# Performance work log

Measured on AMD Instinct MI355X. Metric: run time of the kernel, lower is better.

The kernel has to match this reference:

```python
import jax, jax.numpy as jnp
import numpy as np

NUM_HEADS = 32
NUM_KV_HEADS = 8
HEAD_DIM = 64

def rotate_half(x):
    x1, x2 = jnp.split(x, 2, axis=-1)
    return jnp.concatenate((-x2, x1), axis=-1)

def setup_inputs() -> dict:
    key = jax.random.key(0)
    ks = jax.random.split(key, 7)
    B, S, H = 1, 2048, 2048
    hidden_states = jax.random.normal(ks[0], (B, S, H), dtype=jnp.float32)
    # RoPE tables (llama-style) for positions 0..S-1
    inv_freq = 1.0 / (10000.0 ** (np.arange(0, HEAD_DIM, 2, dtype=np.float32) / HEAD_DIM))
    t = np.arange(S, dtype=np.float32)
    freqs = np.outer(t, inv_freq)              # [S, HEAD_DIM//2]
    emb = np.concatenate([freqs, freqs], axis=-1)  # [S, HEAD_DIM]
    cos = jnp.asarray(np.cos(emb)[None], dtype=jnp.float32)  # [1, S, HEAD_DIM]
    sin = jnp.asarray(np.sin(emb)[None], dtype=jnp.float32)
    sc = 0.02
    Wq = jax.random.normal(ks[1], (H, H), dtype=jnp.float32) * sc
    Wk = jax.random.normal(ks[2], (NUM_KV_HEADS * HEAD_DIM, H), dtype=jnp.float32) * sc
    Wv = jax.random.normal(ks[3], (NUM_KV_HEADS * HEAD_DIM, H), dtype=jnp.float32) * sc
    Wo = jax.random.normal(ks[4], (H, H), dtype=jnp.float32) * sc
    return {"hidden_states": hidden_states, "cos": cos, "sin": sin,
            "Wq": Wq, "Wk": Wk, "Wv": Wv, "Wo": Wo}

def reference(hidden_states, cos, sin, Wq, Wk, Wv, Wo):
    B, S, H = hidden_states.shape
    nh, nkv, hd = NUM_HEADS, NUM_KV_HEADS, HEAD_DIM
    n_rep = nh // nkv
    # projections (torch Linear: x @ W.T)
    q = (hidden_states @ Wq.T).reshape(B, S, nh, hd).transpose(0, 2, 1, 3)   # [B,nh,S,hd]
    k = (hidden_states @ Wk.T).reshape(B, S, nkv, hd).transpose(0, 2, 1, 3)  # [B,nkv,S,hd]
    v = (hidden_states @ Wv.T).reshape(B, S, nkv, hd).transpose(0, 2, 1, 3)
    # RoPE: cos/sin [B,S,hd] -> broadcast over heads
    c = cos[:, None, :, :]
    s = sin[:, None, :, :]
    q = q * c + rotate_half(q) * s
    k = k * c + rotate_half(k) * s
    # GQA: repeat_interleave kv heads
    k = jnp.repeat(k, n_rep, axis=1)  # [B,nh,S,hd]
    v = jnp.repeat(v, n_rep, axis=1)
    # eager attention (NOTE: source applies no causal mask)
    scores = jnp.einsum('bhqd,bhkd->bhqk', q, k) / jnp.sqrt(jnp.float32(hd))
    attn = jax.nn.softmax(scores.astype(jnp.float32), axis=-1).astype(q.dtype)
    out = jnp.einsum('bhqk,bhkd->bhqd', attn, v)          # [B,nh,S,hd]
    out = out.transpose(0, 2, 1, 3).reshape(B, S, nh * hd)
    return out @ Wo.T
```

## Files before the change

kernel.cpp:

```cpp
#include <hip/hip_runtime.h>

typedef __bf16 bf16;
typedef __bf16 bf16x8 __attribute__((ext_vector_type(8)));
typedef __bf16 bf16x4 __attribute__((ext_vector_type(4)));
typedef float f32x4 __attribute__((ext_vector_type(4)));

__device__ __forceinline__ void gload_lds16(const void* g, void* l) {
  __builtin_amdgcn_global_load_lds(
      (const __attribute__((address_space(1))) void*)g,
      (__attribute__((address_space(3))) void*)l, 16, 0, 0);
}

__global__ __launch_bounds__(256) void cast_all(const float* __restrict__ hs,
                                                const float* __restrict__ Wq,
                                                const float* __restrict__ Wk,
                                                const float* __restrict__ Wv,
                                                const float* __restrict__ Wo,
                                                bf16* __restrict__ hsb,
                                                bf16* __restrict__ Wqkv,
                                                bf16* __restrict__ Wob) {
  long i = (long)blockIdx.x * 256 + threadIdx.x;
  const float* s; bf16* d;
  if (i < 1048576)      { s = hs + i * 4;                 d = hsb  + i * 4; }
  else if (i < 2097152) { s = Wq + (i - 1048576) * 4;     d = Wqkv + (i - 1048576) * 4; }
  else if (i < 2359296) { s = Wk + (i - 2097152) * 4;     d = Wqkv + 4194304 + (i - 2097152) * 4; }
  else if (i < 2621440) { s = Wv + (i - 2359296) * 4;     d = Wqkv + 5242880 + (i - 2359296) * 4; }
  else                  { s = Wo + (i - 2621440) * 4;     d = Wob  + (i - 2621440) * 4; }
  float4 v = *(const float4*)s;
  bf16x4 o;
  o[0] = (bf16)v.x; o[1] = (bf16)v.y; o[2] = (bf16)v.z; o[3] = (bf16)v.w;
  *(bf16x4*)d = o;
}

__global__ __launch_bounds__(256) void gemm_qkv(const bf16* __restrict__ A,
                                                const bf16* __restrict__ B,
                                                const float* __restrict__ cosb,
                                                const float* __restrict__ sinb,
                                                bf16* __restrict__ QK,
                                                bf16* __restrict__ Vt_g,
                                                int K) {
  __shared__ bf16 As[2][64][64];
  __shared__ bf16 Bs[2][128][64];
  const int tid  = threadIdx.x;
  const int lane = tid & 63;
  const int w    = tid >> 6;
  const int m0 = blockIdx.y * 64;
  const int n0 = blockIdx.x * 128;
  const int wr = w >> 1, wc = w & 1;
  const int l15 = lane & 15, lq = lane >> 4;

  f32x4 acc[2][4] = {};

  const bf16* Ag = A + (long)(m0 + w * 16 + (lane >> 3)) * K + ((lane & 7) << 3);
  const bf16* Bg = B + (long)(n0 + w * 32 + (lane >> 3)) * K + ((lane & 7) << 3);

#pragma unroll
  for (int i = 0; i < 2; ++i)
    gload_lds16(Ag + (long)i * 8 * K, &As[0][w * 16 + i * 8][0]);
#pragma unroll
  for (int i = 0; i < 4; ++i)
    gload_lds16(Bg + (long)i * 8 * K, &Bs[0][w * 32 + i * 8][0]);
  __syncthreads();

  int cur = 0;
  for (int k0 = 0; k0 < K; k0 += 64) {
    if (k0 + 64 < K) {
#pragma unroll
      for (int i = 0; i < 2; ++i)
        gload_lds16(Ag + (long)i * 8 * K + k0 + 64, &As[cur ^ 1][w * 16 + i * 8][0]);
#pragma unroll
      for (int i = 0; i < 4; ++i)
        gload_lds16(Bg + (long)i * 8 * K + k0 + 64, &Bs[cur ^ 1][w * 32 + i * 8][0]);
    }
#pragma unroll
    for (int kk = 0; kk < 64; kk += 32) {
      bf16x8 a[2], b[4];
#pragma unroll
      for (int m = 0; m < 2; ++m)
        a[m] = *(const bf16x8*)&As[cur][wr * 32 + m * 16 + l15][kk + (lq << 3)];
#pragma unroll
      for (int n = 0; n < 4; ++n)
        b[n] = *(const bf16x8*)&Bs[cur][wc * 64 + n * 16 + l15][kk + (lq << 3)];
#pragma unroll
      for (int m = 0; m < 2; ++m)
#pragma unroll
        for (int n = 0; n < 4; ++n)
          acc[m][n] = __builtin_amdgcn_mfma_f32_16x16x32_bf16(a[m], b[n], acc[m][n], 0, 0, 0);
    }
    __syncthreads();
    cur ^= 1;
  }

  const int rb = m0 + wr * 32 + (lq << 2);
  if (n0 >= 2560) {
    const int cb = n0 + wc * 64 + l15;
#pragma unroll
    for (int m = 0; m < 2; ++m)
#pragma unroll
      for (int n = 0; n < 4; ++n)
#pragma unroll
        for (int j = 0; j < 4; ++j)
          Vt_g[(long)(cb + n * 16 - 2560) * 2048 + (rb + m * 16 + j)] = (bf16)acc[m][n][j];
  } else {
    const int colb = n0 + wc * 64;
    const float scale = (colb >> 6) < 32 ? 0.125f : 1.0f;
#pragma unroll
    for (int m = 0; m < 2; ++m)
#pragma unroll
      for (int j = 0; j < 4; ++j) {
        const int r = rb + m * 16 + j;
        const float* cp = cosb + (long)r * 64;
        const float* sp = sinb + (long)r * 64;
        bf16* qrow = QK + (long)r * 2560 + colb;
#pragma unroll
        for (int n = 0; n < 2; ++n) {
          const int d = n * 16 + l15;
          float c = cp[d], s = sp[d];
          float L = acc[m][n][j], H = acc[m][n + 2][j];
          qrow[d]      = (bf16)((L * c - H * s) * scale);
          qrow[d + 32] = (bf16)((H * c + L * s) * scale);
        }
      }
  }
}

__global__ __launch_bounds__(256) void gemm_bt_f32(const bf16* __restrict__ A,
                                                   const bf16* __restrict__ B,
                                                   float* __restrict__ C,
                                                   int K, int ldc) {
  __shared__ bf16 As[2][64][64];
  __shared__ bf16 Bs[2][128][64];
  const int tid  = threadIdx.x;
  const int lane = tid & 63;
  const int w    = tid >> 6;
  const int m0 = blockIdx.y * 64;
  const int n0 = blockIdx.x * 128;
  const int wr = w >> 1, wc = w & 1;
  const int l15 = lane & 15, lq = lane >> 4;

  f32x4 acc[2][4] = {};

  const bf16* Ag = A + (long)(m0 + w * 16 + (lane >> 3)) * K + ((lane & 7) << 3);
  const bf16* Bg = B + (long)(n0 + w * 32 + (lane >> 3)) * K + ((lane & 7) << 3);

#pragma unroll
  for (int i = 0; i < 2; ++i)
    gload_lds16(Ag + (long)i * 8 * K, &As[0][w * 16 + i * 8][0]);
#pragma unroll
  for (int i = 0; i < 4; ++i)
    gload_lds16(Bg + (long)i * 8 * K, &Bs[0][w * 32 + i * 8][0]);
  __syncthreads();

  int cur = 0;
  for (int k0 = 0; k0 < K; k0 += 64) {
    if (k0 + 64 < K) {
#pragma unroll
      for (int i = 0; i < 2; ++i)
        gload_lds16(Ag + (long)i * 8 * K + k0 + 64, &As[cur ^ 1][w * 16 + i * 8][0]);
#pragma unroll
      for (int i = 0; i < 4; ++i)
        gload_lds16(Bg + (long)i * 8 * K + k0 + 64, &Bs[cur ^ 1][w * 32 + i * 8][0]);
    }
#pragma unroll
    for (int kk = 0; kk < 64; kk += 32) {
      bf16x8 a[2], b[4];
#pragma unroll
      for (int m = 0; m < 2; ++m)
        a[m] = *(const bf16x8*)&As[cur][wr * 32 + m * 16 + l15][kk + (lq << 3)];
#pragma unroll
      for (int n = 0; n < 4; ++n)
        b[n] = *(const bf16x8*)&Bs[cur][wc * 64 + n * 16 + l15][kk + (lq << 3)];
#pragma unroll
      for (int m = 0; m < 2; ++m)
#pragma unroll
        for (int n = 0; n < 4; ++n)
          acc[m][n] = __builtin_amdgcn_mfma_f32_16x16x32_bf16(a[m], b[n], acc[m][n], 0, 0, 0);
    }
    __syncthreads();
    cur ^= 1;
  }

  const int rb = m0 + wr * 32 + (lq << 2);
  const int cb = n0 + wc * 64 + l15;
#pragma unroll
  for (int m = 0; m < 2; ++m)
#pragma unroll
    for (int n = 0; n < 4; ++n)
#pragma unroll
      for (int j = 0; j < 4; ++j)
        C[(long)(rb + m * 16 + j) * ldc + (cb + n * 16)] = acc[m][n][j];
}

__global__ __launch_bounds__(512) void attn_v3(const bf16* __restrict__ QK,
                                               const bf16* __restrict__ Vg,
                                               bf16* __restrict__ O) {
  constexpr int LDT = 72;
  constexpr int LDP = 68;
  __shared__ bf16 Kt[2][64][LDT];
  __shared__ bf16 Vt[2][64][LDT];
  __shared__ bf16 Pl[8][16][LDP];
  const int h   = blockIdx.y;
  const int q0  = blockIdx.x * 128;
  const int kvh = h >> 2;
  const int tid = threadIdx.x, lane = tid & 63, w = tid >> 6;
  const int l15 = lane & 15, lq = lane >> 4;

  const bf16* qptr = QK + (long)(q0 + w * 16 + l15) * 2560 + h * 64 + (lq << 3);
  bf16x8 qf[2];
  qf[0] = *(const bf16x8*)(qptr);
  qf[1] = *(const bf16x8*)(qptr + 32);

  const int sr = tid >> 3;
  const int sc = (tid & 7) << 3;
  const bf16* ksrc = QK + (long)sr * 2560 + 2048 + kvh * 64 + sc;
  const bf16* vsrc = Vg + (long)(kvh * 64 + sr) * 2048 + sc;

  f32x4 oacc[4] = {};
  float lrow[4] = {0.f, 0.f, 0.f, 0.f};

  bf16x8 kreg = *(const bf16x8*)ksrc;
  bf16x8 vreg = *(const bf16x8*)vsrc;

  for (int t = 0; t < 32; ++t) {
    const int b = t & 1;
    *(bf16x8*)&Kt[b][sr][sc] = kreg;
    *(bf16x8*)&Vt[b][sr][sc] = vreg;
    __syncthreads();
    if (t != 31) {
      ksrc += 64 * 2560;
      vsrc += 64;
      kreg = *(const bf16x8*)ksrc;
      vreg = *(const bf16x8*)vsrc;
    }

    f32x4 sacc[4] = {};
#pragma unroll
    for (int kx = 0; kx < 2; ++kx)
#pragma unroll
      for (int nf = 0; nf < 4; ++nf) {
        bf16x8 bb = *(const bf16x8*)&Kt[b][nf * 16 + l15][kx * 32 + (lq << 3)];
        sacc[nf] = __builtin_amdgcn_mfma_f32_16x16x32_bf16(qf[kx], bb, sacc[nf], 0, 0, 0);
      }

#pragma unroll
    for (int nf = 0; nf < 4; ++nf)
#pragma unroll
      for (int j = 0; j < 4; ++j) {
        float pv = __expf(sacc[nf][j]);
        lrow[j] += pv;
        Pl[w][(lq << 2) + j][nf * 16 + l15] = (bf16)pv;
      }

#pragma unroll
    for (int kx = 0; kx < 2; ++kx) {
      bf16x8 a = *(const bf16x8*)&Pl[w][l15][kx * 32 + (lq << 3)];
#pragma unroll
      for (int nf = 0; nf < 4; ++nf) {
        bf16x8 bb = *(const bf16x8*)&Vt[b][nf * 16 + l15][kx * 32 + (lq << 3)];
        oacc[nf] = __builtin_amdgcn_mfma_f32_16x16x32_bf16(a, bb, oacc[nf], 0, 0, 0);
      }
    }
  }

  float ls[4];
#pragma unroll
  for (int j = 0; j < 4; ++j) {
    float v = lrow[j];
#pragma unroll
    for (int off = 1; off < 16; off <<= 1) v += __shfl_xor(v, off, 64);
    ls[j] = v;
  }
#pragma unroll
  for (int nf = 0; nf < 4; ++nf)
#pragma unroll
    for (int j = 0; j < 4; ++j) {
      int r = q0 + w * 16 + (lq << 2) + j;
      int c = h * 64 + nf * 16 + l15;
      O[(long)r * 2048 + c] = (bf16)(oacc[nf][j] / ls[j]);
    }
}

extern "C" void kernel_launch(void* const* d_in, const int* in_sizes, int n_in,
                              void* d_out, int out_size, void* d_ws, size_t ws_size,
                              hipStream_t stream) {
  const float* hs   = (const float*)d_in[0];
  const float* cosb = (const float*)d_in[1];
  const float* sinb = (const float*)d_in[2];
  const float* Wq   = (const float*)d_in[3];
  const float* Wk   = (const float*)d_in[4];
  const float* Wv   = (const float*)d_in[5];
  const float* Wo   = (const float*)d_in[6];
  float* out = (float*)d_out;

  char* ws = (char*)d_ws;
  bf16* hsb   = (bf16*)(ws);
  bf16* Wqkv  = (bf16*)(ws + (8l  << 20));
  bf16* Wob   = (bf16*)(ws + (20l << 20));
  bf16* QKbuf = (bf16*)(ws + (28l << 20));
  bf16* Vt_g  = (bf16*)(ws + (38l << 20));
  bf16* AO    = (bf16*)(ws + (40l << 20));

  cast_all<<<14336, 256, 0, stream>>>(hs, Wq, Wk, Wv, Wo, hsb, Wqkv, Wob);

  gemm_qkv<<<dim3(24, 32), 256, 0, stream>>>(hsb, Wqkv, cosb, sinb, QKbuf, Vt_g, 2048);

  attn_v3<<<dim3(16, 32), 512, 0, stream>>>(QKbuf, Vt_g, AO);

  gemm_bt_f32<<<dim3(16, 32), 256, 0, stream>>>(AO, Wob, out, 2048, 2048);
}
```

Baseline: 247.9 us.

## Rewrite attention with 32x32x16 MFMA and register-resident P via lane shuffles

```diff
diff --git a/kernel.cpp b/kernel.cpp
--- a/kernel.cpp
+++ b/kernel.cpp
@@ -4,11 +4,20 @@
 typedef __bf16 bf16x8 __attribute__((ext_vector_type(8)));
 typedef __bf16 bf16x4 __attribute__((ext_vector_type(4)));
 typedef float f32x4 __attribute__((ext_vector_type(4)));
+typedef float f32x16 __attribute__((ext_vector_type(16)));
+typedef unsigned int u32;
+typedef u32 u32x4 __attribute__((ext_vector_type(4)));
 
 __device__ __forceinline__ void gload_lds16(const void* g, void* l) {
   __builtin_amdgcn_global_load_lds(
       (const __attribute__((address_space(1))) void*)g,
       (__attribute__((address_space(3))) void*)l, 16, 0, 0);
+}
+
+__device__ __forceinline__ u32 pack_bf16(float a, float b) {
+  union { bf16 h; unsigned short s; } ua, ub;
+  ua.h = (bf16)a; ub.h = (bf16)b;
+  return (u32)ua.s | ((u32)ub.s << 16);
 }
 
 __global__ __launch_bounds__(256) void cast_all(const float* __restrict__ hs,
@@ -191,93 +200,123 @@
         C[(long)(rb + m * 16 + j) * ldc + (cb + n * 16)] = acc[m][n][j];
 }
 
-__global__ __launch_bounds__(512) void attn_v3(const bf16* __restrict__ QK,
+__global__ __launch_bounds__(256) void attn_v4(const bf16* __restrict__ QK,
                                                const bf16* __restrict__ Vg,
                                                bf16* __restrict__ O) {
   constexpr int LDT = 72;
-  constexpr int LDP = 68;
   __shared__ bf16 Kt[2][64][LDT];
   __shared__ bf16 Vt[2][64][LDT];
-  __shared__ bf16 Pl[8][16][LDP];
   const int h   = blockIdx.y;
   const int q0  = blockIdx.x * 128;
   const int kvh = h >> 2;
   const int tid = threadIdx.x, lane = tid & 63, w = tid >> 6;
-  const int l15 = lane & 15, lq = lane >> 4;
-
-  const bf16* qptr = QK + (long)(q0 + w * 16 + l15) * 2560 + h * 64 + (lq << 3);
-  bf16x8 qf[2];
-  qf[0] = *(const bf16x8*)(qptr);
-  qf[1] = *(const bf16x8*)(qptr + 32);
+  const int l31 = lane & 31, hi = lane >> 5;
+
+  const bf16* qrow = QK + (long)(q0 + w * 32 + l31) * 2560 + h * 64;
+  bf16x8 qf[4];
+#pragma unroll
+  for (int i = 0; i < 4; ++i)
+    qf[i] = *(const bf16x8*)(qrow + i * 16 + hi * 8);
 
   const int sr = tid >> 3;
   const int sc = (tid & 7) << 3;
   const bf16* ksrc = QK + (long)sr * 2560 + 2048 + kvh * 64 + sc;
   const bf16* vsrc = Vg + (long)(kvh * 64 + sr) * 2048 + sc;
 
-  f32x4 oacc[4] = {};
-  float lrow[4] = {0.f, 0.f, 0.f, 0.f};
-
-  bf16x8 kreg = *(const bf16x8*)ksrc;
-  bf16x8 vreg = *(const bf16x8*)vsrc;
+  f32x16 oacc[2] = {};
+  float lrow = 0.f;
+
+  bf16x8 kreg[2], vreg[2];
+#pragma unroll
+  for (int cc = 0; cc < 2; ++cc) {
+    kreg[cc] = *(const bf16x8*)(ksrc + (long)cc * 32 * 2560);
+    vreg[cc] = *(const bf16x8*)(vsrc + (long)cc * 32 * 2048);
+  }
 
   for (int t = 0; t < 32; ++t) {
     const int b = t & 1;
-    *(bf16x8*)&Kt[b][sr][sc] = kreg;
-    *(bf16x8*)&Vt[b][sr][sc] = vreg;
+#pragma unroll
+    for (int cc = 0; cc < 2; ++cc) {
+      *(bf16x8*)&Kt[b][sr + 32 * cc][sc] = kreg[cc];
+      *(bf16x8*)&Vt[b][sr + 32 * cc][sc] = vreg[cc];
+    }
     __syncthreads();
     if (t != 31) {
       ksrc += 64 * 2560;
       vsrc += 64;
-      kreg = *(const bf16x8*)ksrc;
-      vreg = *(const bf16x8*)vsrc;
-    }
-
-    f32x4 sacc[4] = {};
-#pragma unroll
-    for (int kx = 0; kx < 2; ++kx)
-#pragma unroll
-      for (int nf = 0; nf < 4; ++nf) {
-        bf16x8 bb = *(const bf16x8*)&Kt[b][nf * 16 + l15][kx * 32 + (lq << 3)];
-        sacc[nf] = __builtin_amdgcn_mfma_f32_16x16x32_bf16(qf[kx], bb, sacc[nf], 0, 0, 0);
+#pragma unroll
+      for (int cc = 0; cc < 2; ++cc) {
+        kreg[cc] = *(const bf16x8*)(ksrc + (long)cc * 32 * 2560);
+        vreg[cc] = *(const bf16x8*)(vsrc + (long)cc * 32 * 2048);
       }
-
-#pragma unroll
-    for (int nf = 0; nf < 4; ++nf)
-#pragma unroll
-      for (int j = 0; j < 4; ++j) {
-        float pv = __expf(sacc[nf][j]);
-        lrow[j] += pv;
-        Pl[w][(lq << 2) + j][nf * 16 + l15] = (bf16)pv;
+    }
+
+    f32x16 sacc[2] = {};
+#pragma unroll
+    for (int kb = 0; kb < 2; ++kb)
+#pragma unroll
+      for (int i = 0; i < 4; ++i) {
+        bf16x8 a = *(const bf16x8*)&Kt[b][kb * 32 + l31][i * 16 + hi * 8];
+        sacc[kb] = __builtin_amdgcn_mfma_f32_32x32x16_bf16(a, qf[i], sacc[kb], 0, 0, 0);
       }
 
-#pragma unroll
-    for (int kx = 0; kx < 2; ++kx) {
-      bf16x8 a = *(const bf16x8*)&Pl[w][l15][kx * 32 + (lq << 3)];
-#pragma unroll
-      for (int nf = 0; nf < 4; ++nf) {
-        bf16x8 bb = *(const bf16x8*)&Vt[b][nf * 16 + l15][kx * 32 + (lq << 3)];
-        oacc[nf] = __builtin_amdgcn_mfma_f32_16x16x32_bf16(a, bb, oacc[nf], 0, 0, 0);
+    u32 PK0[8], PK1[8];
+#pragma unroll
+    for (int u = 0; u < 8; ++u) {
+      float p0 = __expf(sacc[0][2 * u]);
+      float p1 = __expf(sacc[0][2 * u + 1]);
+      lrow += p0 + p1;
+      PK0[u] = pack_bf16(p0, p1);
+    }
+#pragma unroll
+    for (int u = 0; u < 8; ++u) {
+      float p0 = __expf(sacc[1][2 * u]);
+      float p1 = __expf(sacc[1][2 * u + 1]);
+      lrow += p0 + p1;
+      PK1[u] = pack_bf16(p0, p1);
+    }
+
+#pragma unroll
+    for (int kj = 0; kj < 4; ++kj) {
+      const int c = kj & 1;
+      u32 o0, o1, o2, o3;
+      if (kj < 2) { o0 = PK0[4*c]; o1 = PK0[4*c+1]; o2 = PK0[4*c+2]; o3 = PK0[4*c+3]; }
+      else        { o0 = PK1[4*c]; o1 = PK1[4*c+1]; o2 = PK1[4*c+2]; o3 = PK1[4*c+3]; }
+      u32 s0 = hi ? o0 : o2;
+      u32 s1 = hi ? o1 : o3;
+      u32 X0 = (u32)__shfl_xor((int)s0, 32, 64);
+      u32 X1 = (u32)__shfl_xor((int)s1, 32, 64);
+      u32x4 bd;
+      bd[0] = hi ? X0 : o0;
+      bd[1] = hi ? X1 : o1;
+      bd[2] = hi ? o2 : X0;
+      bd[3] = hi ? o3 : X1;
+      bf16x8 pb = __builtin_bit_cast(bf16x8, bd);
+#pragma unroll
+      for (int db = 0; db < 2; ++db) {
+        bf16x8 av = *(const bf16x8*)&Vt[b][db * 32 + l31][kj * 16 + hi * 8];
+        oacc[db] = __builtin_amdgcn_mfma_f32_32x32x16_bf16(av, pb, oacc[db], 0, 0, 0);
       }
     }
   }
 
-  float ls[4];
-#pragma unroll
-  for (int j = 0; j < 4; ++j) {
-    float v = lrow[j];
-#pragma unroll
-    for (int off = 1; off < 16; off <<= 1) v += __shfl_xor(v, off, 64);
-    ls[j] = v;
-  }
-#pragma unroll
-  for (int nf = 0; nf < 4; ++nf)
-#pragma unroll
-    for (int j = 0; j < 4; ++j) {
-      int r = q0 + w * 16 + (lq << 2) + j;
-      int c = h * 64 + nf * 16 + l15;
-      O[(long)r * 2048 + c] = (bf16)(oacc[nf][j] / ls[j]);
-    }
+  __syncthreads();
+  float linv = 1.f / (lrow + __shfl_xor(lrow, 32, 64));
+  bf16* ob = (bf16*)&Kt[0][0][0] + w * 32 * 72;
+#pragma unroll
+  for (int db = 0; db < 2; ++db)
+#pragma unroll
+    for (int r = 0; r < 16; ++r) {
+      int d = (r & 3) + 8 * (r >> 2) + 4 * hi + 32 * db;
+      ob[(long)l31 * 72 + d] = (bf16)(oacc[db][r] * linv);
+    }
+#pragma unroll
+  for (int ps = 0; ps < 4; ++ps) {
+    int r = ps * 8 + (lane >> 3);
+    int cch = (lane & 7) << 3;
+    bf16x8 v = *(const bf16x8*)&ob[r * 72 + cch];
+    *(bf16x8*)(O + (long)(q0 + w * 32 + r) * 2048 + h * 64 + cch) = v;
+  }
 }
 
 extern "C" void kernel_launch(void* const* d_in, const int* in_sizes, int n_in,
@@ -304,7 +343,7 @@
 
   gemm_qkv<<<dim3(24, 32), 256, 0, stream>>>(hsb, Wqkv, cosb, sinb, QKbuf, Vt_g, 2048);
 
-  attn_v3<<<dim3(16, 32), 512, 0, stream>>>(QKbuf, Vt_g, AO);
+  attn_v4<<<dim3(16, 32), 256, 0, stream>>>(QKbuf, Vt_g, AO);
 
   gemm_bt_f32<<<dim3(16, 32), 256, 0, stream>>>(AO, Wob, out, 2048, 2048);
 }
```

Result: no change. 244.0 us (-1.6%).
